# Kernel tuning notes

Hardware: AMD Instinct MI355X
Metric: run time of the kernel (lower is better)

The kernel has to match this reference:

```python
import jax, jax.numpy as jnp
import numpy as np

B, S, H, T, E, V, D = 32, 128, 1024, 32, 512, 32000, 256


def setup_inputs() -> dict:
    key = jax.random.key(0)
    ks = jax.random.split(key, 12)
    rn = lambda k, shp, s: jax.random.normal(k, shp, dtype=jnp.float32) * s
    return {
        "fusion_vector": rn(ks[0], (B, S, H), 1.0),
        "hidden_vector": rn(ks[1], (B, H), 1.0),
        "ground_truth_answer_input": rn(ks[2], (B, T, E), 1.0),
        "ground_truth_seq_helper": T,
        "U_w": rn(ks[3], (D, H), 0.02), "U_b": jnp.zeros((D,), jnp.float32),
        "V_w": rn(ks[4], (D, H), 0.02), "V_b": jnp.zeros((D,), jnp.float32),
        "P_w": rn(ks[5], (1, D), 0.02), "P_b": jnp.zeros((1,), jnp.float32),
        "W_ih": rn(ks[6], (3 * H, E + H), 0.02), "b_ih": jnp.zeros((3 * H,), jnp.float32),
        "W_hh": rn(ks[7], (3 * H, H), 0.02), "b_hh": jnp.zeros((3 * H,), jnp.float32),
        "dense_w": rn(ks[8], (V, H), 0.02), "dense_b": jnp.zeros((V,), jnp.float32),
    }


def reference(fusion_vector, hidden_vector, ground_truth_answer_input,
              U_w, U_b, V_w, V_b, P_w, P_b,
              W_ih, b_ih, W_hh, b_hh, dense_w, dense_b,
              ground_truth_seq_helper):
    f = fusion_vector                                  # (B, S, H)
    # V(f) is loop-invariant: precompute tanh(V f) once.
    vf = jnp.tanh(jnp.einsum('bsh,dh->bsd', f, V_w) + V_b)  # (B, S, D)

    def step(h, x):
        # Bilinear attention pooling: q = h (decoder hidden state)
        uh = jnp.tanh(h @ U_w.T + U_b)                 # (B, D)
        scores = jnp.einsum('bsd,d->bs', uh[:, None, :] * vf, P_w[0]) + P_b[0]
        attn = jax.nn.softmax(scores, axis=-1)         # (B, S)
        mix = jnp.einsum('bs,bsh->bh', attn, f)        # (B, H)
        inp = jnp.concatenate([x, mix], axis=1)        # (B, E+H)
        # torch GRUCell: gate order r, z, n
        gx = inp @ W_ih.T + b_ih
        gh = h @ W_hh.T + b_hh
        xr, xz, xn = jnp.split(gx, 3, axis=1)
        hr, hz, hn = jnp.split(gh, 3, axis=1)
        r = jax.nn.sigmoid(xr + hr)
        z = jax.nn.sigmoid(xz + hz)
        n = jnp.tanh(xn + r * hn)
        h_new = (1.0 - z) * n + z * h
        logits = h_new @ dense_w.T + dense_b           # (B, V)
        return h_new, logits

    xs = jnp.swapaxes(ground_truth_answer_input[:, :-1, :], 0, 1)  # (T-1, B, E)
    _, logits = jax.lax.scan(step, hidden_vector, xs)              # (T-1, B, V)
    return jnp.swapaxes(logits, 0, 1)                              # (B, T-1, V)
```

## Files before the change

kernel.cpp:

```cpp
#include <hip/hip_runtime.h>
#include <hip/hip_bf16.h>
#include <math.h>

typedef unsigned short u16;
typedef unsigned long long u64;
typedef __attribute__((ext_vector_type(8))) short short8;
typedef __attribute__((ext_vector_type(4))) float f32x4;
typedef __attribute__((ext_vector_type(2))) _Float16 half2v;

static __device__ __forceinline__ u16 f2b(float x) {
  __hip_bfloat16 h = __float2bfloat16(x);
  return *reinterpret_cast<u16*>(&h);
}
static __device__ __forceinline__ float b2f(u16 u) {
  unsigned int v = ((unsigned int)u) << 16;
  float f;
  __builtin_memcpy(&f, &v, 4);
  return f;
}
static __device__ __forceinline__ u16 f2h(float x) {
  _Float16 h = (_Float16)x;
  u16 u;
  __builtin_memcpy(&u, &h, 2);
  return u;
}
static __device__ __forceinline__ unsigned packh2(float a, float b) {
  return (unsigned)f2h(a) | ((unsigned)f2h(b) << 16);
}
static __device__ __forceinline__ float dot2(unsigned w, unsigned h, float acc) {
  half2v a, b;
  __builtin_memcpy(&a, &w, 4);
  __builtin_memcpy(&b, &h, 4);
#if __has_builtin(__builtin_amdgcn_fdot2)
  return __builtin_amdgcn_fdot2(a, b, acc, false);
#else
  return acc + (float)a[0] * (float)b[0] + (float)a[1] * (float)b[1];
#endif
}

static __device__ __forceinline__ float aldf(const float* p) {
  return __hip_atomic_load(const_cast<float*>(p), __ATOMIC_RELAXED, __HIP_MEMORY_SCOPE_AGENT);
}
static __device__ __forceinline__ void astf(float* p, float v) {
  __hip_atomic_store(p, v, __ATOMIC_RELAXED, __HIP_MEMORY_SCOPE_AGENT);
}
static __device__ __forceinline__ u64 ald8(const u64* p) {
  return __hip_atomic_load(const_cast<u64*>(p), __ATOMIC_RELAXED, __HIP_MEMORY_SCOPE_AGENT);
}
static __device__ __forceinline__ void ast32(unsigned* p, unsigned v) {
  __hip_atomic_store(p, v, __ATOMIC_RELAXED, __HIP_MEMORY_SCOPE_AGENT);
}

__global__ __launch_bounds__(256)
void mega_cvt(const float* __restrict__ f, const float* __restrict__ V_w,
              const float* __restrict__ U_w, const float* __restrict__ W_ih,
              const float* __restrict__ W_hh, const float* __restrict__ dw,
              const float* __restrict__ gt, const float* __restrict__ h0,
              const float* __restrict__ U_b, const float* __restrict__ b_hh,
              u16* __restrict__ fbf, u16* __restrict__ VwB,
              unsigned* __restrict__ WcatH, u16* __restrict__ WxB,
              u16* __restrict__ WmB, u16* __restrict__ dwB,
              u16* __restrict__ Xb, unsigned* __restrict__ hG32,
              float* __restrict__ bcat, unsigned* __restrict__ cnt) {
  const int blk = blockIdx.x, tid = threadIdx.x;
  if (blk < 1600) {
    for (long i = (long)blk * 256 + tid; i < 8192000L; i += 1600L * 256) {
      float4 v = ((const float4*)dw)[i];
      ushort4 o;
      o.x = f2b(v.x); o.y = f2b(v.y); o.z = f2b(v.z); o.w = f2b(v.w);
      ((ushort4*)dwB)[i] = o;
    }
  } else if (blk < 1750) {
    for (long i = (long)(blk - 1600) * 256 + tid; i < 1048576L; i += 150L * 256) {
      float4 v = ((const float4*)f)[i];
      ushort4 o;
      o.x = f2b(v.x); o.y = f2b(v.y); o.z = f2b(v.z); o.w = f2b(v.w);
      ((ushort4*)fbf)[i] = o;
    }
  } else if (blk < 1850) {
    for (long i = (long)(blk - 1750) * 256 + tid; i < 3145728L; i += 100L * 256) {
      long r = i >> 10, c = i & 1023;
      WmB[i] = f2b(W_ih[r * 1536 + 512 + c]);
    }
  } else if (blk < 1920) {
    for (long i = (long)(blk - 1850) * 256 + tid; i < 1572864L; i += 70L * 256) {
      float2 v = ((const float2*)W_hh)[i];
      WcatH[131072 + i] = packh2(v.x, v.y);
    }
  } else if (blk < 1980) {
    for (long i = (long)(blk - 1920) * 256 + tid; i < 1572864L; i += 60L * 256) {
      long r = i >> 9, c = i & 511;
      WxB[i] = f2b(W_ih[r * 1536 + c]);
    }
  } else if (blk < 2000) {
    for (long i = (long)(blk - 1980) * 256 + tid; i < 65536L; i += 20L * 256) {
      float4 v = ((const float4*)V_w)[i];
      ushort4 o;
      o.x = f2b(v.x); o.y = f2b(v.y); o.z = f2b(v.z); o.w = f2b(v.w);
      ((ushort4*)VwB)[i] = o;
    }
  } else if (blk < 2016) {
    for (long i = (long)(blk - 2000) * 256 + tid; i < 131072L; i += 16L * 256) {
      float2 v = ((const float2*)U_w)[i];
      WcatH[i] = packh2(v.x, v.y);
    }
  } else if (blk < 2040) {
    for (long i = (long)(blk - 2016) * 256 + tid; i < 524288L; i += 24L * 256) {
      long m = i >> 9;
      int k = (int)(i & 511);
      Xb[i] = (m < 992) ? f2b(gt[((m & 31) * 32 + (m >> 5)) * 512 + k]) : (u16)0;
    }
  } else {
    int b0 = blk - 2040;
    for (long i = (long)b0 * 256 + tid; i < 16384L; i += 8L * 256) {
      float2 v = ((const float2*)h0)[i];
      hG32[i] = packh2(v.x, v.y);
    }
    for (int i = b0 * 256 + tid; i < 3328; i += 8 * 256)
      bcat[i] = (i < 256) ? U_b[i] : b_hh[i - 256];
    if (b0 == 0 && tid < 64) cnt[tid] = 0;
  }
}

template<int EPI>
__global__ __launch_bounds__(256)
void gemm_bt(const u16* __restrict__ A, const u16* __restrict__ B,
             void* __restrict__ C0,
             const float* __restrict__ bias, const float* __restrict__ pw,
             int M, int N, int K) {
  __shared__ u16 As[4096];
  __shared__ u16 Bs[4096];
  const int tid = threadIdx.x;
  const int lane = tid & 63, wid = tid >> 6;

  int gx = gridDim.x, gy = gridDim.y;
  int orig = blockIdx.y * gx + blockIdx.x;
  int G = gx < 8 ? gx : 8;
  int ng = gx / G;
  int full = ng * G * gy;
  int ct, rt;
  if (orig < full) {
    int grp = orig / (G * gy), rem = orig % (G * gy);
    ct = grp * G + rem % G;
    rt = rem / G;
  } else {
    int Gt = gx - ng * G;
    int rem = orig - full;
    ct = ng * G + rem % Gt;
    rt = rem / Gt;
  }
  const long row0 = (long)rt * 128;
  const long col0 = (long)ct * 128;

  const int wm = (wid >> 1) * 64, wn = (wid & 1) * 64;
  const int fr = lane & 15, fq = lane >> 4;
  const int sr = wid * 16 + (lane >> 2);
  const int sc = (lane & 3) * 8;

  const u16* Ag0 = A + (row0 + sr) * (long)K + sc;
  const u16* Ag1 = Ag0 + 64 * (long)K;
  const u16* Bg0 = B + (col0 + sr) * (long)K + sc;
  const u16* Bg1 = Bg0 + 64 * (long)K;

  u16* AsW0 = &As[wid * 512];
  u16* AsW1 = &As[2048 + wid * 512];
  u16* BsW0 = &Bs[wid * 512];
  u16* BsW1 = &Bs[2048 + wid * 512];

  f32x4 acc[4][4];
#pragma unroll
  for (int i = 0; i < 4; ++i)
#pragma unroll
    for (int j = 0; j < 4; ++j) acc[i][j] = {0.f, 0.f, 0.f, 0.f};

  for (int k0 = 0; k0 < K; k0 += 32) {
    __builtin_amdgcn_global_load_lds((const __attribute__((address_space(1))) void*)(Ag0 + k0),
                                     (__attribute__((address_space(3))) void*)AsW0, 16, 0, 0);
    __builtin_amdgcn_global_load_lds((const __attribute__((address_space(1))) void*)(Ag1 + k0),
                                     (__attribute__((address_space(3))) void*)AsW1, 16, 0, 0);
    __builtin_amdgcn_global_load_lds((const __attribute__((address_space(1))) void*)(Bg0 + k0),
                                     (__attribute__((address_space(3))) void*)BsW0, 16, 0, 0);
    __builtin_amdgcn_global_load_lds((const __attribute__((address_space(1))) void*)(Bg1 + k0),
                                     (__attribute__((address_space(3))) void*)BsW1, 16, 0, 0);
    __syncthreads();
    short8 af[4], bfv[4];
#pragma unroll
    for (int i = 0; i < 4; ++i) af[i] = *(const short8*)&As[(wm + i * 16 + fr) * 32 + fq * 8];
#pragma unroll
    for (int i = 0; i < 4; ++i) bfv[i] = *(const short8*)&Bs[(wn + i * 16 + fr) * 32 + fq * 8];
#pragma unroll
    for (int i = 0; i < 4; ++i)
#pragma unroll
      for (int j = 0; j < 4; ++j)
        acc[i][j] = __builtin_amdgcn_mfma_f32_16x16x32_bf16(af[i], bfv[j], acc[i][j], 0, 0, 0);
    __syncthreads();
  }

#pragma unroll
  for (int i = 0; i < 4; ++i)
#pragma unroll
    for (int j = 0; j < 4; ++j)
#pragma unroll
      for (int q = 0; q < 4; ++q) {
        long gr = row0 + wm + i * 16 + fq * 4 + q;
        long gc = col0 + wn + j * 16 + fr;
        float v = acc[i][j][q];
        if constexpr (EPI == 0) {
          ((u16*)C0)[gr * (long)N + gc] = f2b(v);
        } else if constexpr (EPI == 1) {
          ((u16*)C0)[gr * (long)N + gc] = f2b(tanhf(v + bias[gc]) * pw[gc]);
        } else if constexpr (EPI == 2) {
          if (gr < M) ((float*)C0)[gr * (long)N + gc] = v + bias[gc];
        } else {
          if (gr < M) {
            long bb = gr & 31, tt = gr >> 5;
            float o = v + bias[gc];
            __builtin_nontemporal_store(o, &((float*)C0)[(bb * 31 + tt) * (long)N + gc]);
          }
        }
      }
}

__global__ __launch_bounds__(1024)
void persist(const unsigned* __restrict__ WcatH, const float* __restrict__ bcat,
             const u16* __restrict__ wvfb, const u16* __restrict__ FWb,
             const float* __restrict__ GX, const float* __restrict__ pbv,
             const float* __restrict__ h0,
             unsigned* __restrict__ hG32, float* __restrict__ gates,
             u16* __restrict__ Hbuf, unsigned* __restrict__ cnt) {
  const int tid = threadIdx.x;
  const int blk = blockIdx.x;
  const int rg = blk >> 2, bg = blk & 3;
  const int b = blk >> 3, jc = blk & 7;

  __shared__ unsigned wlds[52 * 516];
  __shared__ float hl2[128];
  __shared__ __align__(16) char smem[45056];
  unsigned* hlds = (unsigned*)smem;
  float*    plds = (float*)(smem + 16512);
  float* uhl   = (float*)smem;
  float* part  = uhl + 256;
  float* attnv = part + 1024;
  float* gmp   = attnv + 128;

  const float pb0 = pbv[0];
  if (tid < 128) hl2[tid] = h0[b * 1024 + jc * 128 + tid];

  for (int it = tid; it < 52 * 512; it += 1024) {
    int row = it >> 9, idx = it & 511;
    wlds[row * 516 + idx] = WcatH[(long)(rg * 52 + row) * 512 + idx];
  }

  auto xbar = [&](unsigned target) {
    __syncthreads();
    if (tid == 0) {
      __hip_atomic_fetch_add(cnt, 1u, __ATOMIC_RELAXED, __HIP_MEMORY_SCOPE_AGENT);
      while (__hip_atomic_load(cnt, __ATOMIC_RELAXED, __HIP_MEMORY_SCOPE_AGENT) < target) {
        __builtin_amdgcn_s_sleep(2);
      }
    }
    __syncthreads();
  };
  xbar(256u);

  for (int t = 0; t < 31; ++t) {
    {
      long base = (long)(bg * 8) * 512;
      int g = tid * 4;
      u64 v0 = ald8((const u64*)(hG32 + base + g));
      u64 v1 = ald8((const u64*)(hG32 + base + g + 2));
      int bi = g >> 9, idx = g & 511;
      unsigned* dst = hlds + bi * 516 + idx;
      dst[0] = (unsigned)v0; dst[1] = (unsigned)(v0 >> 32);
      dst[2] = (unsigned)v1; dst[3] = (unsigned)(v1 >> 32);
    }
    __syncthreads();
    {
      const int akc = tid >> 6, w = tid & 63;
      const int bl = w & 7, rch = w >> 3;
      uint4 hv[8];
      const uint4* hp = (const uint4*)(hlds + bl * 516 + akc * 32);
#pragma unroll
      for (int j = 0; j < 8; ++j) hv[j] = hp[j];
#pragma unroll
      for (int i = 0; i < 7; ++i) {
        int rl = rch * 7 + i;
        if (rl < 52) {
          const uint4* wp = (const uint4*)(wlds + rl * 516 + akc * 32);
          float acc = 0.f;
#pragma unroll
          for (int j = 0; j < 8; ++j) {
            uint4 w4 = wp[j];
            acc = dot2(w4.x, hv[j].x, acc);
            acc = dot2(w4.y, hv[j].y, acc);
            acc = dot2(w4.z, hv[j].z, acc);
            acc = dot2(w4.w, hv[j].w, acc);
          }
          plds[(rl * 8 + bl) * 17 + akc] = acc;
        }
      }
    }
    __syncthreads();
    if (tid < 416) {
      const float* pp = plds + tid * 17;
      float s = 0.f;
#pragma unroll
      for (int k = 0; k < 16; ++k) s += pp[k];
      int rl = tid >> 3, bl = tid & 7;
      astf(gates + (long)(bg * 8 + bl) * 3328 + rg * 52 + rl, s);
    }
    xbar(256u * (2 * t + 2));

    if (tid < 128) {
      u64 v = ald8((const u64*)(gates + (long)b * 3328 + tid * 2));
      float2 f2v;
      __builtin_memcpy(&f2v, &v, 8);
      uhl[tid * 2] = tanhf(f2v.x + bcat[tid * 2]);
      uhl[tid * 2 + 1] = tanhf(f2v.y + bcat[tid * 2 + 1]);
    }
    __syncthreads();
    {
      const int s = tid & 127, q = tid >> 7;
      const u16* wr = wvfb + ((long)(b * 128 + s)) * 256 + q * 32;
      const float* uq = &uhl[q * 32];
      float p = 0.f;
#pragma unroll
      for (int d = 0; d < 32; d += 8) {
        short8 wv = *(const short8*)(wr + d);
#pragma unroll
        for (int e = 0; e < 8; ++e) p += b2f((u16)wv[e]) * uq[d + e];
      }
      part[tid] = p;
    }
    __syncthreads();
    if (tid < 128) {
      float s8 = pb0;
#pragma unroll
      for (int j = 0; j < 8; ++j) s8 += part[tid + 128 * j];
      attnv[tid] = s8;
    }
    __syncthreads();
    if (tid < 64) {
      float m = fmaxf(attnv[tid], attnv[tid + 64]);
#pragma unroll
      for (int o = 32; o; o >>= 1) m = fmaxf(m, __shfl_xor(m, o));
      float e0 = expf(attnv[tid] - m), e1 = expf(attnv[tid + 64] - m);
      float s2 = e0 + e1;
#pragma unroll
      for (int o = 32; o; o >>= 1) s2 += __shfl_xor(s2, o);
      float inv = 1.f / s2;
      attnv[tid] = e0 * inv;
      attnv[tid + 64] = e1 * inv;
    }
    __syncthreads();
    {
      const int ml = tid & 127, sh = tid >> 7;
      const int col = jc * 128 + ml;
      float g0 = 0.f, g1 = 0.f, g2 = 0.f;
      const u16* fw = FWb + ((long)(b * 128 + sh * 16)) * 3072 + col;
#pragma unroll 4
      for (int s = 0; s < 16; ++s) {
        float a = attnv[sh * 16 + s];
        g0 += a * b2f(fw[0]);
        g1 += a * b2f(fw[1024]);
        g2 += a * b2f(fw[2048]);
        fw += 3072;
      }
      gmp[0 * 1024 + tid] = g0;
      gmp[1 * 1024 + tid] = g1;
      gmp[2 * 1024 + tid] = g2;
    }
    __syncthreads();
    if (tid < 128) {
      const int m = jc * 128 + tid;
      float gm0 = 0.f, gm1 = 0.f, gm2 = 0.f;
#pragma unroll
      for (int j = 0; j < 8; ++j) {
        gm0 += gmp[0 * 1024 + tid + 128 * j];
        gm1 += gmp[1 * 1024 + tid + 128 * j];
        gm2 += gmp[2 * 1024 + tid + 128 * j];
      }
      float gh0 = aldf(gates + (long)b * 3328 + 256 + m) + bcat[256 + m];
      float gh1 = aldf(gates + (long)b * 3328 + 1280 + m) + bcat[1280 + m];
      float gh2 = aldf(gates + (long)b * 3328 + 2304 + m) + bcat[2304 + m];
      const long gxo = ((long)t * 32 + b) * 3072;
      float xr = GX[gxo + m] + gm0;
      float xz = GX[gxo + 1024 + m] + gm1;
      float xn = GX[gxo + 2048 + m] + gm2;
      float r = 1.f / (1.f + expf(-(xr + gh0)));
      float z = 1.f / (1.f + expf(-(xz + gh1)));
      float n = tanhf(xn + r * gh2);
      float h2 = (1.f - z) * n + z * hl2[tid];
      hl2[tid] = h2;
      Hbuf[((long)t * 32 + b) * 1024 + m] = f2b(h2);
      float hp = __shfl_xor(h2, 1);
      if ((tid & 1) == 0) {
        unsigned pk = (unsigned)f2h(h2) | ((unsigned)f2h(hp) << 16);
        ast32(hG32 + (long)b * 512 + jc * 64 + (tid >> 1), pk);
      }
    }
    xbar(256u * (2 * t + 3));
  }
}


extern "C" void kernel_launch(void* const* d_in, const int* in_sizes, int n_in,
                              void* d_out, int out_size, void* d_ws, size_t ws_size,
                              hipStream_t stream) {
  const float* f    = (const float*)d_in[0];
  const float* h0   = (const float*)d_in[1];
  const float* gt   = (const float*)d_in[2];
  const float* U_w  = (const float*)d_in[4];
  const float* U_b  = (const float*)d_in[5];
  const float* V_w  = (const float*)d_in[6];
  const float* V_b  = (const float*)d_in[7];
  const float* P_w  = (const float*)d_in[8];
  const float* P_b  = (const float*)d_in[9];
  const float* W_ih = (const float*)d_in[10];
  const float* b_ih = (const float*)d_in[11];
  const float* W_hh = (const float*)d_in[12];
  const float* b_hh = (const float*)d_in[13];
  const float* dw   = (const float*)d_in[14];
  const float* db   = (const float*)d_in[15];

  char* w = (char*)d_ws;
  auto alloc = [&](size_t bytes) { char* p = w; w += (bytes + 255) & ~255ULL; return p; };

  u16*      fbf   = (u16*)alloc(4096L * 1024 * 2);
  u16*      VwB   = (u16*)alloc(256L * 1024 * 2);
  unsigned* WcatH = (unsigned*)alloc(3328L * 512 * 4);
  u16*      WxB   = (u16*)alloc(3072L * 512 * 2);
  u16*      WmB   = (u16*)alloc(3072L * 1024 * 2);
  u16*      dwB   = (u16*)alloc(32000L * 1024 * 2);
  u16*      Xb    = (u16*)alloc(1024L * 512 * 2);
  u16*      wvfb  = (u16*)alloc(4096L * 256 * 2);
  float*    GX    = (float*)alloc(1024L * 3072 * 4);
  u16*      FWb   = (u16*)alloc(4096L * 3072 * 2);
  unsigned* hG32  = (unsigned*)alloc(32L * 512 * 4);
  float*    gates = (float*)alloc(32L * 3328 * 4);
  u16*      Hbuf  = (u16*)alloc(1024L * 1024 * 2);
  float*    bcat  = (float*)alloc(3328L * 4);
  unsigned* cnt   = (unsigned*)alloc(256);

  mega_cvt<<<2048, 256, 0, stream>>>(f, V_w, U_w, W_ih, W_hh, dw, gt, h0, U_b, b_hh,
                                     fbf, VwB, WcatH, WxB, WmB, dwB, Xb, hG32,
                                     bcat, cnt);

  gemm_bt<1><<<dim3(2, 32), 256, 0, stream>>>(fbf, VwB, wvfb, V_b, P_w, 4096, 256, 1024);
  gemm_bt<2><<<dim3(24, 8), 256, 0, stream>>>(Xb, WxB, GX, b_ih, nullptr, 992, 3072, 512);
  gemm_bt<0><<<dim3(24, 32), 256, 0, stream>>>(fbf, WmB, FWb, nullptr, nullptr, 4096, 3072, 1024);

  {
    void* ka[] = {(void*)&WcatH, (void*)&bcat, (void*)&wvfb, (void*)&FWb,
                  (void*)&GX,    (void*)&P_b,  (void*)&h0,   (void*)&hG32,
                  (void*)&gates, (void*)&Hbuf, (void*)&cnt};
    hipLaunchCooperativeKernel((void*)persist, dim3(256), dim3(1024), ka, 0, stream);
  }

  gemm_bt<3><<<dim3(250, 8), 256, 0, stream>>>(Hbuf, dwB, (float*)d_out, db, nullptr,
                                               992, 32000, 1024);
}
```

Measured before the change: 805.0 us.

## Use bf16 MFMA for recurrent gate matvec in persistent kernel

Recurrent weights (U_w, W_hh) and the shared hidden state are now stored as bf16 instead of packed fp16. The per-step hidden-to-gate product moves from per-thread fdot2 loops with an LDS partial-sum reduction to 16x16x32 bf16 MFMA on four waves, padding the unused batch columns from a zero buffer. This removes the partial-sum buffer, one barrier and the reduction pass from every timestep. In exchange, twelve of the sixteen waves sit idle during the matvec, half the MFMA columns are wasted, and bf16 gives lower mantissa precision than fp16 for the hidden state.

```diff
diff --git a/kernel.cpp b/kernel.cpp
--- a/kernel.cpp
+++ b/kernel.cpp
@@ -6,7 +6,6 @@
 typedef unsigned long long u64;
 typedef __attribute__((ext_vector_type(8))) short short8;
 typedef __attribute__((ext_vector_type(4))) float f32x4;
-typedef __attribute__((ext_vector_type(2))) _Float16 half2v;
 
 static __device__ __forceinline__ u16 f2b(float x) {
   __hip_bfloat16 h = __float2bfloat16(x);
@@ -18,24 +17,8 @@
   __builtin_memcpy(&f, &v, 4);
   return f;
 }
-static __device__ __forceinline__ u16 f2h(float x) {
-  _Float16 h = (_Float16)x;
-  u16 u;
-  __builtin_memcpy(&u, &h, 2);
-  return u;
-}
-static __device__ __forceinline__ unsigned packh2(float a, float b) {
-  return (unsigned)f2h(a) | ((unsigned)f2h(b) << 16);
-}
-static __device__ __forceinline__ float dot2(unsigned w, unsigned h, float acc) {
-  half2v a, b;
-  __builtin_memcpy(&a, &w, 4);
-  __builtin_memcpy(&b, &h, 4);
-#if __has_builtin(__builtin_amdgcn_fdot2)
-  return __builtin_amdgcn_fdot2(a, b, acc, false);
-#else
-  return acc + (float)a[0] * (float)b[0] + (float)a[1] * (float)b[1];
-#endif
+static __device__ __forceinline__ unsigned packb2(float a, float b) {
+  return (unsigned)f2b(a) | ((unsigned)f2b(b) << 16);
 }
 
 static __device__ __forceinline__ float aldf(const float* p) {
@@ -46,6 +29,9 @@
 }
 static __device__ __forceinline__ u64 ald8(const u64* p) {
   return __hip_atomic_load(const_cast<u64*>(p), __ATOMIC_RELAXED, __HIP_MEMORY_SCOPE_AGENT);
+}
+static __device__ __forceinline__ unsigned ald32(const unsigned* p) {
+  return __hip_atomic_load(const_cast<unsigned*>(p), __ATOMIC_RELAXED, __HIP_MEMORY_SCOPE_AGENT);
 }
 static __device__ __forceinline__ void ast32(unsigned* p, unsigned v) {
   __hip_atomic_store(p, v, __ATOMIC_RELAXED, __HIP_MEMORY_SCOPE_AGENT);
@@ -58,7 +44,7 @@
               const float* __restrict__ gt, const float* __restrict__ h0,
               const float* __restrict__ U_b, const float* __restrict__ b_hh,
               u16* __restrict__ fbf, u16* __restrict__ VwB,
-              unsigned* __restrict__ WcatH, u16* __restrict__ WxB,
+              u16* __restrict__ WcatB, u16* __restrict__ WxB,
               u16* __restrict__ WmB, u16* __restrict__ dwB,
               u16* __restrict__ Xb, unsigned* __restrict__ hG32,
               float* __restrict__ bcat, unsigned* __restrict__ cnt) {
@@ -83,9 +69,11 @@
       WmB[i] = f2b(W_ih[r * 1536 + 512 + c]);
     }
   } else if (blk < 1920) {
-    for (long i = (long)(blk - 1850) * 256 + tid; i < 1572864L; i += 70L * 256) {
-      float2 v = ((const float2*)W_hh)[i];
-      WcatH[131072 + i] = packh2(v.x, v.y);
+    for (long i = (long)(blk - 1850) * 256 + tid; i < 786432L; i += 70L * 256) {
+      float4 v = ((const float4*)W_hh)[i];
+      ushort4 o;
+      o.x = f2b(v.x); o.y = f2b(v.y); o.z = f2b(v.z); o.w = f2b(v.w);
+      ((ushort4*)WcatB)[65536 + i] = o;
     }
   } else if (blk < 1980) {
     for (long i = (long)(blk - 1920) * 256 + tid; i < 1572864L; i += 60L * 256) {
@@ -100,9 +88,11 @@
       ((ushort4*)VwB)[i] = o;
     }
   } else if (blk < 2016) {
-    for (long i = (long)(blk - 2000) * 256 + tid; i < 131072L; i += 16L * 256) {
-      float2 v = ((const float2*)U_w)[i];
-      WcatH[i] = packh2(v.x, v.y);
+    for (long i = (long)(blk - 2000) * 256 + tid; i < 65536L; i += 16L * 256) {
+      float4 v = ((const float4*)U_w)[i];
+      ushort4 o;
+      o.x = f2b(v.x); o.y = f2b(v.y); o.z = f2b(v.z); o.w = f2b(v.w);
+      ((ushort4*)WcatB)[i] = o;
     }
   } else if (blk < 2040) {
     for (long i = (long)(blk - 2016) * 256 + tid; i < 524288L; i += 24L * 256) {
@@ -114,7 +104,7 @@
     int b0 = blk - 2040;
     for (long i = (long)b0 * 256 + tid; i < 16384L; i += 8L * 256) {
       float2 v = ((const float2*)h0)[i];
-      hG32[i] = packh2(v.x, v.y);
+      hG32[i] = packb2(v.x, v.y);
     }
     for (int i = b0 * 256 + tid; i < 3328; i += 8 * 256)
       bcat[i] = (i < 256) ? U_b[i] : b_hh[i - 256];
@@ -222,7 +212,7 @@
 }
 
 __global__ __launch_bounds__(1024)
-void persist(const unsigned* __restrict__ WcatH, const float* __restrict__ bcat,
+void persist(const u16* __restrict__ WcatB, const float* __restrict__ bcat,
              const u16* __restrict__ wvfb, const u16* __restrict__ FWb,
              const float* __restrict__ GX, const float* __restrict__ pbv,
              const float* __restrict__ h0,
@@ -233,11 +223,11 @@
   const int rg = blk >> 2, bg = blk & 3;
   const int b = blk >> 3, jc = blk & 7;
 
-  __shared__ unsigned wlds[52 * 516];
+  __shared__ __align__(16) u16 wlds[52 * 1032];
+  __shared__ __align__(16) u16 zbuf[32];
   __shared__ float hl2[128];
-  __shared__ __align__(16) char smem[45056];
-  unsigned* hlds = (unsigned*)smem;
-  float*    plds = (float*)(smem + 16512);
+  __shared__ __align__(16) char smem[18432];
+  u16*   hlds  = (u16*)smem;
   float* uhl   = (float*)smem;
   float* part  = uhl + 256;
   float* attnv = part + 1024;
@@ -245,10 +235,12 @@
 
   const float pb0 = pbv[0];
   if (tid < 128) hl2[tid] = h0[b * 1024 + jc * 128 + tid];
+  if (tid < 32) zbuf[tid] = 0;
 
   for (int it = tid; it < 52 * 512; it += 1024) {
     int row = it >> 9, idx = it & 511;
-    wlds[row * 516 + idx] = WcatH[(long)(rg * 52 + row) * 512 + idx];
+    *(unsigned*)&wlds[row * 1032 + idx * 2] =
+        ((const unsigned*)WcatB)[(long)(rg * 52 + row) * 512 + idx];
   }
 
   auto xbar = [&](unsigned target) {
@@ -264,50 +256,37 @@
   xbar(256u);
 
   for (int t = 0; t < 31; ++t) {
+    for (int i = tid; i < 4096; i += 1024) {
+      int bi = i >> 9, idx = i & 511;
+      unsigned v = ald32(hG32 + (long)(bg * 8 + bi) * 512 + idx);
+      *(unsigned*)&hlds[bi * 1032 + idx * 2] = v;
+    }
+    __syncthreads();
     {
-      long base = (long)(bg * 8) * 512;
-      int g = tid * 4;
-      u64 v0 = ald8((const u64*)(hG32 + base + g));
-      u64 v1 = ald8((const u64*)(hG32 + base + g + 2));
-      int bi = g >> 9, idx = g & 511;
-      unsigned* dst = hlds + bi * 516 + idx;
-      dst[0] = (unsigned)v0; dst[1] = (unsigned)(v0 >> 32);
-      dst[2] = (unsigned)v1; dst[3] = (unsigned)(v1 >> 32);
-    }
-    __syncthreads();
-    {
-      const int akc = tid >> 6, w = tid & 63;
-      const int bl = w & 7, rch = w >> 3;
-      uint4 hv[8];
-      const uint4* hp = (const uint4*)(hlds + bl * 516 + akc * 32);
-#pragma unroll
-      for (int j = 0; j < 8; ++j) hv[j] = hp[j];
-#pragma unroll
-      for (int i = 0; i < 7; ++i) {
-        int rl = rch * 7 + i;
-        if (rl < 52) {
-          const uint4* wp = (const uint4*)(wlds + rl * 516 + akc * 32);
-          float acc = 0.f;
-#pragma unroll
-          for (int j = 0; j < 8; ++j) {
-            uint4 w4 = wp[j];
-            acc = dot2(w4.x, hv[j].x, acc);
-            acc = dot2(w4.y, hv[j].y, acc);
-            acc = dot2(w4.z, hv[j].z, acc);
-            acc = dot2(w4.w, hv[j].w, acc);
+      const int wv = tid >> 6, lane = tid & 63;
+      if (wv < 4) {
+        const int fr = lane & 15, fq = lane >> 4;
+        int arow = wv * 16 + fr;
+        if (arow >= 52) arow = 0;
+        const u16* ap = wlds + arow * 1032 + fq * 8;
+        const u16* bp = (fr < 8) ? (hlds + fr * 1032 + fq * 8) : (zbuf + fq * 8);
+        const int bstep = (fr < 8) ? 32 : 0;
+        f32x4 acc = {0.f, 0.f, 0.f, 0.f};
+#pragma unroll
+        for (int kt = 0; kt < 32; ++kt) {
+          short8 av = *(const short8*)(ap + kt * 32);
+          short8 bv = *(const short8*)(bp + kt * bstep);
+          acc = __builtin_amdgcn_mfma_f32_16x16x32_bf16(av, bv, acc, 0, 0, 0);
+        }
+        if (fr < 8) {
+          const long gbase = (long)(bg * 8 + fr) * 3328 + rg * 52;
+#pragma unroll
+          for (int q = 0; q < 4; ++q) {
+            int row = wv * 16 + fq * 4 + q;
+            if (row < 52) astf(gates + gbase + row, acc[q]);
           }
-          plds[(rl * 8 + bl) * 17 + akc] = acc;
         }
       }
-    }
-    __syncthreads();
-    if (tid < 416) {
-      const float* pp = plds + tid * 17;
-      float s = 0.f;
-#pragma unroll
-      for (int k = 0; k < 16; ++k) s += pp[k];
-      int rl = tid >> 3, bl = tid & 7;
-      astf(gates + (long)(bg * 8 + bl) * 3328 + rg * 52 + rl, s);
     }
     xbar(256u * (2 * t + 2));
 
@@ -395,7 +374,7 @@
       Hbuf[((long)t * 32 + b) * 1024 + m] = f2b(h2);
       float hp = __shfl_xor(h2, 1);
       if ((tid & 1) == 0) {
-        unsigned pk = (unsigned)f2h(h2) | ((unsigned)f2h(hp) << 16);
+        unsigned pk = packb2(h2, hp);
         ast32(hG32 + (long)b * 512 + jc * 64 + (tid >> 1), pk);
       }
     }
@@ -428,7 +407,7 @@
 
   u16*      fbf   = (u16*)alloc(4096L * 1024 * 2);
   u16*      VwB   = (u16*)alloc(256L * 1024 * 2);
-  unsigned* WcatH = (unsigned*)alloc(3328L * 512 * 4);
+  u16*      WcatB = (u16*)alloc(3328L * 1024 * 2);
   u16*      WxB   = (u16*)alloc(3072L * 512 * 2);
   u16*      WmB   = (u16*)alloc(3072L * 1024 * 2);
   u16*      dwB   = (u16*)alloc(32000L * 1024 * 2);
@@ -443,7 +422,7 @@
   unsigned* cnt   = (unsigned*)alloc(256);
 
   mega_cvt<<<2048, 256, 0, stream>>>(f, V_w, U_w, W_ih, W_hh, dw, gt, h0, U_b, b_hh,
-                                     fbf, VwB, WcatH, WxB, WmB, dwB, Xb, hG32,
+                                     fbf, VwB, WcatB, WxB, WmB, dwB, Xb, hG32,
                                      bcat, cnt);
 
   gemm_bt<1><<<dim3(2, 32), 256, 0, stream>>>(fbf, VwB, wvfb, V_b, P_w, 4096, 256, 1024);
@@ -451,7 +430,7 @@
   gemm_bt<0><<<dim3(24, 32), 256, 0, stream>>>(fbf, WmB, FWb, nullptr, nullptr, 4096, 3072, 1024);
 
   {
-    void* ka[] = {(void*)&WcatH, (void*)&bcat, (void*)&wvfb, (void*)&FWb,
+    void* ka[] = {(void*)&WcatB, (void*)&bcat, (void*)&wvfb, (void*)&FWb,
                   (void*)&GX,    (void*)&P_b,  (void*)&h0,   (void*)&hG32,
                   (void*)&gates, (void*)&Hbuf, (void*)&cnt};
     hipLaunchCooperativeKernel((void*)persist, dim3(256), dim3(1024), ka, 0, stream);
```

After: 895.4 us. 1.11x slower.
